# Kernel optimization log

Measured on AMD Instinct MI355X. Metric: run time of the kernel, lower is better.

Reference implementation:

```python
import jax, jax.numpy as jnp
import numpy as np
from jax import lax

DIM = 1024
DIM_INNER = 2048  # int(dim * expansion_factor)


def log_g(x):
    # log-space g(x): where(x>=0, log(relu(x)+0.5), -softplus(-x))
    return jnp.where(x >= 0, jnp.log(jax.nn.relu(x) + 0.5), -jax.nn.softplus(-x))


def heinsen_associative_scan_log(log_coeffs, log_values):
    # parallel log-space linear recurrence over the sequence axis (axis=1)
    a_star = jnp.cumsum(log_coeffs, axis=1)
    log_h0_plus_b_star = lax.cumlogsumexp(log_values - a_star, axis=1)
    return a_star + log_h0_plus_b_star


def setup_inputs() -> dict:
    key = jax.random.key(0)
    k_x, k_w1, k_w2 = jax.random.split(key, 3)
    x = jax.random.normal(k_x, (4, 4096, DIM), dtype=jnp.float32)
    # Linear(dim, 2*dim_inner, bias=False): store as [in, out] for x @ W
    W_hg = jax.random.normal(k_w1, (DIM, 2 * DIM_INNER), dtype=jnp.float32) * (1.0 / np.sqrt(DIM))
    W_out = jax.random.normal(k_w2, (DIM_INNER, DIM), dtype=jnp.float32) * (1.0 / np.sqrt(DIM_INNER))
    return {"x": x, "W_hg": W_hg, "W_out": W_out}


def reference(x, W_hg, W_out):
    # x: [b, s, dim]
    hg = jnp.einsum('bsd,de->bse', x, W_hg)  # [b, s, 2*dim_inner]
    hidden, gate = jnp.split(hg, 2, axis=-1)
    log_coeffs = -jax.nn.softplus(gate)        # log(1 - z)
    log_z = -jax.nn.softplus(-gate)            # log z
    log_values = log_z + log_g(hidden)
    log_h = heinsen_associative_scan_log(log_coeffs, log_values)  # [b, s, dim_inner]
    out = jnp.exp(log_h)
    return jnp.einsum('bse,ed->bsd', out, W_out)
```

## Files before the change

### kernel.cpp

```cpp
#include <hip/hip_runtime.h>
#include <cmath>

#define DIM 1024
#define DIM_INNER 2048
#define BATCH 4
#define SEQ 4096
#define MTOT (BATCH * SEQ)
#define CHUNK 32
#define NCHUNK (SEQ / CHUNK)

typedef __bf16 bf16x8 __attribute__((ext_vector_type(8)));
typedef short short8_t __attribute__((ext_vector_type(8)));
typedef float floatx4 __attribute__((ext_vector_type(4)));
typedef unsigned short u16x4 __attribute__((ext_vector_type(4)));
typedef unsigned int uint4_t __attribute__((ext_vector_type(4)));
typedef float float4_t __attribute__((ext_vector_type(4)));
typedef unsigned short ushort_t;

__device__ __forceinline__ unsigned short f2bf(float f) {
  unsigned int u = __builtin_bit_cast(unsigned int, f);
  u += 0x7fffu + ((u >> 16) & 1u);
  return (unsigned short)(u >> 16);
}
__device__ __forceinline__ float bflo2f(unsigned int u) {
  return __builtin_bit_cast(float, u << 16);
}
__device__ __forceinline__ float bfhi2f(unsigned int u) {
  return __builtin_bit_cast(float, u & 0xffff0000u);
}

__device__ __forceinline__ void lclv_fast(float h, float g, float& lc, float& lv) {
  float eg = __expf(-fabsf(g));
  float sp = fmaxf(g, 0.f) + __logf(1.f + eg);
  lc = -sp;
  float eh = __expf(h);
  float t  = (h >= 0.f) ? (h + 0.5f) : (1.f + eh);
  float lt = __logf(t);
  float lg = (h >= 0.f) ? lt : (h - lt);
  lv = g + lc + lg;
}
__device__ __forceinline__ float logaddexp_f(float a, float b) {
  float m = fmaxf(a, b);
  return m + __logf(1.f + __expf(-fabsf(a - b)));
}

__device__ __forceinline__ void async_copy16(const ushort_t* g, ushort_t* l) {
  __builtin_amdgcn_global_load_lds(
      (const __attribute__((address_space(1))) void*)g,
      (__attribute__((address_space(3))) void*)l, 16, 0, 0);
}

__global__ __launch_bounds__(256) void convert_f32_bf16(
    const float* __restrict__ src, ushort_t* __restrict__ dst) {
  int i = blockIdx.x * 256 + threadIdx.x;
  float4 v = ((const float4*)src)[i];
  u16x4 o = {f2bf(v.x), f2bf(v.y), f2bf(v.z), f2bf(v.w)};
  ((u16x4*)dst)[i] = o;
}

__global__ __launch_bounds__(256) void transpose_f32_bf16(
    const float* __restrict__ src, ushort_t* __restrict__ dst, int K, int N) {
  __shared__ float tile[32][33];
  int tx = threadIdx.x & 31, ty = threadIdx.x >> 5;
  int n0 = blockIdx.x * 32, k0 = blockIdx.y * 32;
#pragma unroll
  for (int i = 0; i < 4; i++) {
    int k = ty + i * 8;
    tile[k][tx] = src[(size_t)(k0 + k) * N + n0 + tx];
  }
  __syncthreads();
#pragma unroll
  for (int i = 0; i < 4; i++) {
    int r = ty + i * 8;
    dst[(size_t)(n0 + r) * K + k0 + tx] = f2bf(tile[tx][r]);
  }
}

__global__ __launch_bounds__(256) void gemm1_fused(
    const ushort_t* __restrict__ Xbf, const ushort_t* __restrict__ Wt,
    unsigned int* __restrict__ LCLV) {
  __shared__ __align__(16) ushort_t As[128 * 32];
  __shared__ __align__(16) ushort_t Bh[64 * 32];
  __shared__ __align__(16) ushort_t Bg[64 * 32];

  const int tid = threadIdx.x;
  const int wave = tid >> 6;
  const int lane = tid & 63;
  const int n0 = blockIdx.x * 64;
  const int m0 = blockIdx.y * 128;
  const int l15 = lane & 15;
  const int quad = lane >> 4;
  const int wr = wave >> 1, wc = wave & 1;
  const int lrow = lane >> 2;
  const int lkof = (lane & 3) * 8;

  floatx4 acch[4][2], accg[4][2];
#pragma unroll
  for (int i = 0; i < 4; i++)
#pragma unroll
    for (int j = 0; j < 2; j++) {
      acch[i][j] = (floatx4){0.f, 0.f, 0.f, 0.f};
      accg[i][j] = (floatx4){0.f, 0.f, 0.f, 0.f};
    }

  for (int k0 = 0; k0 < DIM; k0 += 32) {
    __syncthreads();
    async_copy16(Xbf + (size_t)(m0 + wave * 16 + lrow) * DIM + k0 + lkof,
                 As + wave * 512);
    async_copy16(Xbf + (size_t)(m0 + (wave + 4) * 16 + lrow) * DIM + k0 + lkof,
                 As + (wave + 4) * 512);
    async_copy16(Wt + (size_t)(n0 + wave * 16 + lrow) * DIM + k0 + lkof,
                 Bh + wave * 512);
    async_copy16(Wt + (size_t)(n0 + DIM_INNER + wave * 16 + lrow) * DIM + k0 + lkof,
                 Bg + wave * 512);
    __syncthreads();

    bf16x8 af[4], bhf[2], bgf[2];
#pragma unroll
    for (int i = 0; i < 4; i++) {
      short8_t sa = *(const short8_t*)(As + (size_t)(wr * 64 + i * 16 + l15) * 32 + quad * 8);
      af[i] = __builtin_bit_cast(bf16x8, sa);
    }
#pragma unroll
    for (int j = 0; j < 2; j++) {
      short8_t sh = *(const short8_t*)(Bh + (size_t)(wc * 32 + j * 16 + l15) * 32 + quad * 8);
      bhf[j] = __builtin_bit_cast(bf16x8, sh);
      short8_t sg = *(const short8_t*)(Bg + (size_t)(wc * 32 + j * 16 + l15) * 32 + quad * 8);
      bgf[j] = __builtin_bit_cast(bf16x8, sg);
    }
#pragma unroll
    for (int i = 0; i < 4; i++)
#pragma unroll
      for (int j = 0; j < 2; j++) {
        acch[i][j] = __builtin_amdgcn_mfma_f32_16x16x32_bf16(af[i], bhf[j], acch[i][j], 0, 0, 0);
        accg[i][j] = __builtin_amdgcn_mfma_f32_16x16x32_bf16(af[i], bgf[j], accg[i][j], 0, 0, 0);
      }
  }

#pragma unroll
  for (int i = 0; i < 4; i++)
#pragma unroll
    for (int j = 0; j < 2; j++) {
      int col = n0 + wc * 32 + j * 16 + l15;
#pragma unroll
      for (int r = 0; r < 4; r++) {
        int row = m0 + wr * 64 + i * 16 + quad * 4 + r;
        float lc, lv;
        lclv_fast(acch[i][j][r], accg[i][j][r], lc, lv);
        unsigned int pk = ((unsigned int)f2bf(lv) << 16) | (unsigned int)f2bf(lc);
        LCLV[(size_t)row * DIM_INNER + col] = pk;
      }
    }
}

__global__ __launch_bounds__(256) void scan_phase1(
    const unsigned int* __restrict__ LCLV,
    float* __restrict__ Asum, float* __restrict__ Lend, int nbch) {
  const int EQ = DIM_INNER / 4;
  int tid = blockIdx.x * 256 + threadIdx.x;
  int ep = tid % EQ;
  int tmp = tid / EQ;
  int c = tmp % NCHUNK;
  int bz = tmp / NCHUNK;
  size_t base4 = ((size_t)bz * SEQ + (size_t)c * CHUNK) * EQ + ep;
  const uint4_t* L4 = (const uint4_t*)LCLV;

  float4_t asum = {0.f, 0.f, 0.f, 0.f};
  float4_t logh = {-INFINITY, -INFINITY, -INFINITY, -INFINITY};
#pragma unroll 4
  for (int t = 0; t < CHUNK; t++) {
    uint4_t u = L4[base4 + (size_t)t * EQ];
#pragma unroll
    for (int k = 0; k < 4; k++) {
      float lc = bflo2f(u[k]), lv = bfhi2f(u[k]);
      asum[k] += lc;
      logh[k] = logaddexp_f(lc + logh[k], lv);
    }
  }
  size_t sidx = ((size_t)c * nbch + (size_t)bz * DIM_INNER) / 4 + ep;
  ((float4_t*)Asum)[sidx] = asum;
  ((float4_t*)Lend)[sidx] = logh;
}

__global__ __launch_bounds__(256) void scan_phase2(
    float* Asum, const float* __restrict__ Lend, int nbch) {
  int ch = blockIdx.x * 256 + threadIdx.x;
  float p = -INFINITY;
  for (int c = 0; c < NCHUNK; c++) {
    float a = Asum[(size_t)c * nbch + ch];
    float le = Lend[(size_t)c * nbch + ch];
    Asum[(size_t)c * nbch + ch] = p;
    p = logaddexp_f(a + p, le);
  }
}

__global__ __launch_bounds__(256) void scan_phase3(
    const unsigned int* __restrict__ LCLV, const float* __restrict__ P,
    ushort_t* __restrict__ H, int nbch) {
  const int EQ = DIM_INNER / 4;
  int tid = blockIdx.x * 256 + threadIdx.x;
  int ep = tid % EQ;
  int tmp = tid / EQ;
  int c = tmp % NCHUNK;
  int bz = tmp / NCHUNK;
  size_t base4 = ((size_t)bz * SEQ + (size_t)c * CHUNK) * EQ + ep;
  const uint4_t* L4 = (const uint4_t*)LCLV;
  u16x4* H4 = (u16x4*)H;

  size_t pidx = ((size_t)c * nbch + (size_t)bz * DIM_INNER) / 4 + ep;
  float4_t logh = ((const float4_t*)P)[pidx];
#pragma unroll 4
  for (int t = 0; t < CHUNK; t++) {
    uint4_t u = L4[base4 + (size_t)t * EQ];
    u16x4 hv;
#pragma unroll
    for (int k = 0; k < 4; k++) {
      float lc = bflo2f(u[k]), lv = bfhi2f(u[k]);
      logh[k] = logaddexp_f(lc + logh[k], lv);
      hv[k] = f2bf(__expf(logh[k]));
    }
    H4[base4 + (size_t)t * EQ] = hv;
  }
}

__global__ __launch_bounds__(256) void gemm2(
    const ushort_t* __restrict__ Hbf, const ushort_t* __restrict__ Wot,
    float* __restrict__ OUT) {
  __shared__ __align__(16) ushort_t As[128 * 32];
  __shared__ __align__(16) ushort_t Bs[128 * 32];

  const int tid = threadIdx.x;
  const int wave = tid >> 6;
  const int lane = tid & 63;
  const int n0 = blockIdx.x * 128;
  const int m0 = blockIdx.y * 128;
  const int l15 = lane & 15;
  const int quad = lane >> 4;
  const int wr = wave >> 1, wc = wave & 1;
  const int lrow = lane >> 2;
  const int lkof = (lane & 3) * 8;

  floatx4 acc[4][4];
#pragma unroll
  for (int i = 0; i < 4; i++)
#pragma unroll
    for (int j = 0; j < 4; j++) acc[i][j] = (floatx4){0.f, 0.f, 0.f, 0.f};

  for (int k0 = 0; k0 < DIM_INNER; k0 += 32) {
    __syncthreads();
#pragma unroll
    for (int p = 0; p < 2; p++) {
      int u = wave + p * 4;
      async_copy16(Hbf + (size_t)(m0 + u * 16 + lrow) * DIM_INNER + k0 + lkof,
                   As + u * 512);
      async_copy16(Wot + (size_t)(n0 + u * 16 + lrow) * DIM_INNER + k0 + lkof,
                   Bs + u * 512);
    }
    __syncthreads();

    bf16x8 af[4], bf[4];
#pragma unroll
    for (int i = 0; i < 4; i++) {
      short8_t sa = *(const short8_t*)(As + (size_t)(wr * 64 + i * 16 + l15) * 32 + quad * 8);
      af[i] = __builtin_bit_cast(bf16x8, sa);
      short8_t sb = *(const short8_t*)(Bs + (size_t)(wc * 64 + i * 16 + l15) * 32 + quad * 8);
      bf[i] = __builtin_bit_cast(bf16x8, sb);
    }
#pragma unroll
    for (int i = 0; i < 4; i++)
#pragma unroll
      for (int j = 0; j < 4; j++)
        acc[i][j] = __builtin_amdgcn_mfma_f32_16x16x32_bf16(af[i], bf[j], acc[i][j], 0, 0, 0);
  }

#pragma unroll
  for (int i = 0; i < 4; i++)
#pragma unroll
    for (int j = 0; j < 4; j++) {
      int col = n0 + wc * 64 + j * 16 + l15;
#pragma unroll
      for (int r = 0; r < 4; r++) {
        int row = m0 + wr * 64 + i * 16 + quad * 4 + r;
        OUT[(size_t)row * DIM + col] = acc[i][j][r];
      }
    }
}

extern "C" void kernel_launch(void* const* d_in, const int* in_sizes, int n_in,
                              void* d_out, int out_size, void* d_ws, size_t ws_size,
                              hipStream_t stream) {
  const float* X = (const float*)d_in[0];
  const float* Whg = (const float*)d_in[1];
  const float* Wout = (const float*)d_in[2];
  float* out = (float*)d_out;

  ushort_t* Xbf = (ushort_t*)d_ws;
  ushort_t* Whg_t = Xbf + (size_t)MTOT * DIM;
  ushort_t* Wout_t = Whg_t + (size_t)(2 * DIM_INNER) * DIM;
  char* pp = (char*)(Wout_t + (size_t)DIM * DIM_INNER);

  const size_t fixed_bytes = (size_t)MTOT * DIM * 2 +
                             (size_t)2 * DIM_INNER * DIM * 2 +
                             (size_t)DIM * DIM_INNER * 2;
  const size_t per_batch = (size_t)SEQ * DIM_INNER * 4 +
                           (size_t)SEQ * DIM_INNER * 2 +
                           2 * (size_t)DIM_INNER * NCHUNK * 4;
  int nb = 4;
  while (nb > 1 && fixed_bytes + (size_t)nb * per_batch > ws_size) nb >>= 1;
  const int npass = BATCH / nb;

  convert_f32_bf16<<<(MTOT * DIM / 4) / 256, 256, 0, stream>>>(X, Xbf);
  transpose_f32_bf16<<<dim3(2 * DIM_INNER / 32, DIM / 32), 256, 0, stream>>>(
      Whg, Whg_t, DIM, 2 * DIM_INNER);
  transpose_f32_bf16<<<dim3(DIM / 32, DIM_INNER / 32), 256, 0, stream>>>(
      Wout, Wout_t, DIM_INNER, DIM);

  for (int pass = 0; pass < npass; pass++) {
    const int b0 = pass * nb;
    const int nrows = nb * SEQ;
    const int nbch = nb * DIM_INNER;

    unsigned int* LCLV = (unsigned int*)pp;
    ushort_t* Hbf = (ushort_t*)(LCLV + (size_t)nb * SEQ * DIM_INNER);
    float* Asum = (float*)(Hbf + (size_t)nb * SEQ * DIM_INNER);
    float* Lend = Asum + (size_t)nb * DIM_INNER * NCHUNK;

    gemm1_fused<<<dim3(DIM_INNER / 64, nrows / 128), 256, 0, stream>>>(
        Xbf + (size_t)b0 * SEQ * DIM, Whg_t, LCLV);
    scan_phase1<<<(nbch / 4 * NCHUNK) / 256, 256, 0, stream>>>(LCLV, Asum, Lend, nbch);
    scan_phase2<<<nbch / 256, 256, 0, stream>>>(Asum, Lend, nbch);
    scan_phase3<<<(nbch / 4 * NCHUNK) / 256, 256, 0, stream>>>(LCLV, Asum, Hbf, nbch);
    gemm2<<<dim3(DIM / 128, nrows / 128), 256, 0, stream>>>(
        Hbf, Wout_t, out + (size_t)b0 * SEQ * DIM);
  }
}
```

Measured before the change: 508.5 us.

## Rewrite gemm1 with 256x128 tiles, swizzled LDS and multi-buffered async pipeline

The fused hidden/gate GEMM now uses 512-thread blocks with a 256x(64h+64g) tile and BK=64. A and B tiles sit in XOR-swizzled LDS, with triple buffering for A and double buffering for B. Global async copies for upcoming k-tiles are interleaved with four MFMA quarter-phases, each bracketed by barriers and s_setprio. The aim is more data reuse per LDS load, fewer bank conflicts, and memory latency hidden behind compute, at the cost of larger LDS use (160KB), more registers and intricate waitcnt/barrier correctness.

```diff
diff --git a/kernel.cpp b/kernel.cpp
--- a/kernel.cpp
+++ b/kernel.cpp
@@ -76,77 +76,161 @@
   }
 }
 
-__global__ __launch_bounds__(256) void gemm1_fused(
+#define G1_BK 64
+#define G1_NT (DIM / G1_BK)
+
+__global__ __launch_bounds__(512, 2) void gemm1_fused(
     const ushort_t* __restrict__ Xbf, const ushort_t* __restrict__ Wt,
     unsigned int* __restrict__ LCLV) {
-  __shared__ __align__(16) ushort_t As[128 * 32];
-  __shared__ __align__(16) ushort_t Bh[64 * 32];
-  __shared__ __align__(16) ushort_t Bg[64 * 32];
+  __shared__ __align__(16) ushort_t lds[81920];
 
   const int tid = threadIdx.x;
-  const int wave = tid >> 6;
+  const int wv = tid >> 6;
   const int lane = tid & 63;
-  const int n0 = blockIdx.x * 64;
-  const int m0 = blockIdx.y * 128;
+  const int wr = wv >> 2;
+  const int wc = wv & 3;
   const int l15 = lane & 15;
   const int quad = lane >> 4;
-  const int wr = wave >> 1, wc = wave & 1;
-  const int lrow = lane >> 2;
-  const int lkof = (lane & 3) * 8;
-
-  floatx4 acch[4][2], accg[4][2];
-#pragma unroll
-  for (int i = 0; i < 4; i++)
-#pragma unroll
-    for (int j = 0; j < 2; j++) {
-      acch[i][j] = (floatx4){0.f, 0.f, 0.f, 0.f};
-      accg[i][j] = (floatx4){0.f, 0.f, 0.f, 0.f};
-    }
-
-  for (int k0 = 0; k0 < DIM; k0 += 32) {
-    __syncthreads();
-    async_copy16(Xbf + (size_t)(m0 + wave * 16 + lrow) * DIM + k0 + lkof,
-                 As + wave * 512);
-    async_copy16(Xbf + (size_t)(m0 + (wave + 4) * 16 + lrow) * DIM + k0 + lkof,
-                 As + (wave + 4) * 512);
-    async_copy16(Wt + (size_t)(n0 + wave * 16 + lrow) * DIM + k0 + lkof,
-                 Bh + wave * 512);
-    async_copy16(Wt + (size_t)(n0 + DIM_INNER + wave * 16 + lrow) * DIM + k0 + lkof,
-                 Bg + wave * 512);
-    __syncthreads();
-
-    bf16x8 af[4], bhf[2], bgf[2];
-#pragma unroll
-    for (int i = 0; i < 4; i++) {
-      short8_t sa = *(const short8_t*)(As + (size_t)(wr * 64 + i * 16 + l15) * 32 + quad * 8);
-      af[i] = __builtin_bit_cast(bf16x8, sa);
-    }
-#pragma unroll
-    for (int j = 0; j < 2; j++) {
-      short8_t sh = *(const short8_t*)(Bh + (size_t)(wc * 32 + j * 16 + l15) * 32 + quad * 8);
-      bhf[j] = __builtin_bit_cast(bf16x8, sh);
-      short8_t sg = *(const short8_t*)(Bg + (size_t)(wc * 32 + j * 16 + l15) * 32 + quad * 8);
-      bgf[j] = __builtin_bit_cast(bf16x8, sg);
-    }
-#pragma unroll
-    for (int i = 0; i < 4; i++)
-#pragma unroll
-      for (int j = 0; j < 2; j++) {
-        acch[i][j] = __builtin_amdgcn_mfma_f32_16x16x32_bf16(af[i], bhf[j], acch[i][j], 0, 0, 0);
-        accg[i][j] = __builtin_amdgcn_mfma_f32_16x16x32_bf16(af[i], bgf[j], accg[i][j], 0, 0, 0);
-      }
-  }
-
-#pragma unroll
-  for (int i = 0; i < 4; i++)
+  const int n0 = blockIdx.x * 128;
+  const int m0 = blockIdx.y * 256;
+
+  floatx4 acc[8][4];
+#pragma unroll
+  for (int i = 0; i < 8; i++)
+#pragma unroll
+    for (int j = 0; j < 4; j++) acc[i][j] = (floatx4){0.f, 0.f, 0.f, 0.f};
+
+  bf16x8 aF[4][2], bF[2][2];
+
+  auto stageA = [&](int kt, int half, int buf) {
+#pragma unroll
+    for (int L = 0; L < 2; L++) {
+      int e = L * 512 + tid;
+      int row = e >> 3, slot = e & 7;
+      const ushort_t* src = Xbf + (size_t)(m0 + half * 128 + row) * DIM +
+                            kt * 64 + ((slot ^ (row & 7)) << 3);
+      async_copy16(src, lds + (buf * 2 + half) * 8192 + e * 8);
+    }
+  };
+  auto stageB = [&](int kt, int half, int buf) {
+#pragma unroll
+    for (int L = 0; L < 2; L++) {
+      int e = L * 512 + tid;
+      int row = e >> 3, slot = e & 7;
+      int br = half * 128 + row;
+      int grow = n0 + ((br >> 6) << 5) + (br & 31) + ((br & 32) ? DIM_INNER : 0);
+      const ushort_t* src = Wt + (size_t)grow * DIM +
+                            kt * 64 + ((slot ^ (row & 7)) << 3);
+      async_copy16(src, lds + 49152 + (buf * 2 + half) * 8192 + e * 8);
+    }
+  };
+  auto readA = [&](int buf, int mf, int ks) -> bf16x8 {
+    int r = mf * 16 + l15;
+    const ushort_t* p = lds + (buf * 2 + wr) * 8192 + r * 64 +
+                        ((((ks << 2) | quad) ^ (r & 7)) << 3);
+    return __builtin_bit_cast(bf16x8, *(const short8_t*)p);
+  };
+  auto readB = [&](int buf, int nf, int ks) -> bf16x8 {
+    int br = wc * 64 + nf * 16 + l15;
+    int half = br >> 7, r = br & 127;
+    const ushort_t* p = lds + 49152 + (buf * 2 + half) * 8192 + r * 64 +
+                        ((((ks << 2) | quad) ^ (r & 7)) << 3);
+    return __builtin_bit_cast(bf16x8, *(const short8_t*)p);
+  };
+  auto mmaQ = [&](int mb, int nb) {
+#pragma unroll
+    for (int mf = 0; mf < 4; mf++)
+#pragma unroll
+      for (int nf = 0; nf < 2; nf++)
+#pragma unroll
+        for (int ks = 0; ks < 2; ks++)
+          acc[mb + mf][nb + nf] = __builtin_amdgcn_mfma_f32_16x16x32_bf16(
+              aF[mf][ks], bF[nf][ks], acc[mb + mf][nb + nf], 0, 0, 0);
+  };
+
+  stageA(0, 0, 0); stageA(0, 1, 0);
+  stageB(0, 0, 0); stageB(0, 1, 0);
+  stageA(1, 0, 1); stageA(1, 1, 1);
+  asm volatile("s_waitcnt vmcnt(4)" ::: "memory");
+  __builtin_amdgcn_s_barrier();
+
+  int bufA = 0, bufB = 0, bufAn = 2, bufBn = 1;
+  for (int u = 0; u < G1_NT; u++) {
+    const int kb = (u + 1 < G1_NT) ? u + 1 : G1_NT - 1;
+    const int ka = (u + 2 < G1_NT) ? u + 2 : G1_NT - 1;
+
+#pragma unroll
+    for (int mf = 0; mf < 4; mf++)
+#pragma unroll
+      for (int ks = 0; ks < 2; ks++) aF[mf][ks] = readA(bufA, mf, ks);
+#pragma unroll
+    for (int nf = 0; nf < 2; nf++)
+#pragma unroll
+      for (int ks = 0; ks < 2; ks++) bF[nf][ks] = readB(bufB, nf, ks);
+    stageB(kb, 0, bufBn);
+    __builtin_amdgcn_s_barrier();
+    asm volatile("s_waitcnt lgkmcnt(0)" ::: "memory");
+    __builtin_amdgcn_sched_barrier(0);
+    __builtin_amdgcn_s_setprio(1);
+    mmaQ(0, 0);
+    __builtin_amdgcn_s_setprio(0);
+    __builtin_amdgcn_s_barrier();
+
+#pragma unroll
+    for (int nf = 0; nf < 2; nf++)
+#pragma unroll
+      for (int ks = 0; ks < 2; ks++) bF[nf][ks] = readB(bufB, nf + 2, ks);
+    stageB(kb, 1, bufBn);
+    __builtin_amdgcn_s_barrier();
+    asm volatile("s_waitcnt lgkmcnt(0)" ::: "memory");
+    __builtin_amdgcn_sched_barrier(0);
+    __builtin_amdgcn_s_setprio(1);
+    mmaQ(0, 2);
+    __builtin_amdgcn_s_setprio(0);
+    __builtin_amdgcn_s_barrier();
+
+#pragma unroll
+    for (int mf = 0; mf < 4; mf++)
+#pragma unroll
+      for (int ks = 0; ks < 2; ks++) aF[mf][ks] = readA(bufA, mf + 4, ks);
+    stageA(ka, 0, bufAn);
+    __builtin_amdgcn_s_barrier();
+    asm volatile("s_waitcnt lgkmcnt(0)" ::: "memory");
+    __builtin_amdgcn_sched_barrier(0);
+    __builtin_amdgcn_s_setprio(1);
+    mmaQ(4, 2);
+    __builtin_amdgcn_s_setprio(0);
+    __builtin_amdgcn_s_barrier();
+
+#pragma unroll
+    for (int nf = 0; nf < 2; nf++)
+#pragma unroll
+      for (int ks = 0; ks < 2; ks++) bF[nf][ks] = readB(bufB, nf, ks);
+    stageA(ka, 1, bufAn);
+    asm volatile("s_waitcnt vmcnt(4)" ::: "memory");
+    __builtin_amdgcn_s_barrier();
+    asm volatile("s_waitcnt lgkmcnt(0)" ::: "memory");
+    __builtin_amdgcn_sched_barrier(0);
+    __builtin_amdgcn_s_setprio(1);
+    mmaQ(4, 0);
+    __builtin_amdgcn_s_setprio(0);
+    __builtin_amdgcn_s_barrier();
+
+    bufA = (bufA == 2) ? 0 : bufA + 1;
+    bufAn = (bufAn == 2) ? 0 : bufAn + 1;
+    bufB ^= 1; bufBn ^= 1;
+  }
+
+#pragma unroll
+  for (int mf = 0; mf < 8; mf++)
 #pragma unroll
     for (int j = 0; j < 2; j++) {
       int col = n0 + wc * 32 + j * 16 + l15;
 #pragma unroll
       for (int r = 0; r < 4; r++) {
-        int row = m0 + wr * 64 + i * 16 + quad * 4 + r;
+        int row = m0 + wr * 128 + mf * 16 + quad * 4 + r;
         float lc, lv;
-        lclv_fast(acch[i][j][r], accg[i][j][r], lc, lv);
+        lclv_fast(acc[mf][j][r], acc[mf][j + 2][r], lc, lv);
         unsigned int pk = ((unsigned int)f2bf(lv) << 16) | (unsigned int)f2bf(lc);
         LCLV[(size_t)row * DIM_INNER + col] = pk;
       }
@@ -325,7 +409,7 @@
     float* Asum = (float*)(Hbf + (size_t)nb * SEQ * DIM_INNER);
     float* Lend = Asum + (size_t)nb * DIM_INNER * NCHUNK;
 
-    gemm1_fused<<<dim3(DIM_INNER / 64, nrows / 128), 256, 0, stream>>>(
+    gemm1_fused<<<dim3(DIM_INNER / 128, nrows / 256), 512, 0, stream>>>(
         Xbf + (size_t)b0 * SEQ * DIM, Whg_t, LCLV);
     scan_phase1<<<(nbch / 4 * NCHUNK) / 256, 256, 0, stream>>>(LCLV, Asum, Lend, nbch);
     scan_phase2<<<nbch / 256, 256, 0, stream>>>(Asum, Lend, nbch);
```

After: 493.0 us. -3.0%, faster.
